# Optimization experiments

Hardware: AMD Instinct MI355X
Metric: run time of the kernel (lower is better)

Reference implementation:

```python
import jax, jax.numpy as jnp
import numpy as np
import math

B, S = 2, 2048
D_IN = 512
D_OUT = 512
P = 8
K = 8


def setup_inputs() -> dict:
    key = jax.random.key(0)
    ks = jax.random.split(key, 8)
    mean_phi = math.log(math.sqrt(2.0 / (D_IN * K)))
    mean_w2 = math.log(math.sqrt(2.0 / D_OUT))
    x = jax.random.normal(ks[0], (B, S, D_IN), dtype=jnp.float32)
    phi_raw = mean_phi + 0.2 * jax.random.normal(ks[1], (D_OUT, D_IN * K), dtype=jnp.float32)
    phi_bias = jnp.zeros((D_OUT,), dtype=jnp.float32)
    raw_weight2 = mean_w2 + 0.2 * jax.random.normal(ks[2], (P, D_OUT, D_OUT), dtype=jnp.float32)
    bias2 = jnp.zeros((P, D_OUT), dtype=jnp.float32)
    gate_raw2 = jnp.full((P,), -3.0, dtype=jnp.float32)
    # kaiming_uniform with a=sqrt(5) on shape (P, 2*D_in, D_out): fan_in = 2*D_in
    bound = math.sqrt(6.0 / ((1.0 + 5.0) * (2 * D_IN)))
    z_weight = jax.random.uniform(ks[3], (P, 2 * D_IN, D_OUT), dtype=jnp.float32,
                                  minval=-bound, maxval=bound)
    gate_raw = jnp.full((P,), -3.0, dtype=jnp.float32)
    output_bias = jnp.zeros((P, D_OUT), dtype=jnp.float32)
    return {
        "x": x, "phi_raw": phi_raw, "phi_bias": phi_bias,
        "raw_weight2": raw_weight2, "bias2": bias2, "gate_raw2": gate_raw2,
        "z_weight": z_weight, "gate_raw": gate_raw, "output_bias": output_bias,
    }


def reference(x, phi_raw, phi_bias, raw_weight2, bias2, gate_raw2,
              z_weight, gate_raw, output_bias):
    sp = jax.nn.softplus
    orig = x.shape
    x_flat = x.reshape(-1, D_IN)                              # [N, Din]
    N = x_flat.shape[0]
    shifts = jnp.linspace(-1.0, 1.0, K, dtype=x.dtype)        # [k]
    phi = sp(x_flat[:, :, None] + shifts[None, None, :])      # [N, Din, k]
    phi_flat = phi.reshape(N, D_IN * K)                       # [N, Din*k]
    # PositiveLinearHK: weight = softplus(raw)^2
    w_phi = jnp.square(sp(phi_raw))                           # [Dout, Din*k]
    x_proj = phi_flat @ w_phi.T + phi_bias                    # [N, Dout]
    g1 = jax.nn.sigmoid(gate_raw)[:, None, None]              # [P,1,1]
    z0 = sp(x_proj[None, :, :] * g1)                          # [P, N, Dout]
    w2 = jnp.square(sp(raw_weight2))                          # [P, Dout, Dout]
    # bmm(z0, w2.transpose(1,2)) == einsum over the second Dout axis of w2
    z1 = jnp.einsum('pnd,ped->pne', z0, w2) + bias2[:, None, :]
    g2 = jax.nn.sigmoid(gate_raw2)[:, None, None]
    z1 = sp(z1 * g2)                                          # [P, N, Dout]
    x_res_in = jnp.concatenate([x_flat, x_flat], axis=-1)     # [N, 2*Din]
    x_res = jnp.einsum('nc,pce->pne', x_res_in, z_weight)     # [P, N, Dout]
    z_final = sp(z1 + x_res) + output_bias[:, None, :]        # [P, N, Dout]
    out = jnp.transpose(z_final, (1, 0, 2))                   # [N, P, Dout]
    return out.reshape(tuple(orig[:-1]) + (P, D_OUT))
```

## Files before the change

### kernel.cpp

```cpp
#include <hip/hip_runtime.h>

typedef unsigned short u16;
typedef __attribute__((ext_vector_type(8))) short bf16x8;
typedef __attribute__((ext_vector_type(4))) float floatx4;
typedef __attribute__((ext_vector_type(8))) unsigned short u16x8;
typedef __attribute__((ext_vector_type(4))) unsigned short u16x4;

#define NTOK 4096
#define DDIN 512
#define DDOUT 512
#define NP 8

__device__ __forceinline__ float b2f(u16 b) {
    union { unsigned int u; float f; } v; v.u = ((unsigned int)b) << 16; return v.f;
}
__device__ __forceinline__ u16 f2b(float f) {
    union { float f; unsigned int u; } v; v.f = f;
    unsigned int r = (v.u + 0x7fffu + ((v.u >> 16) & 1u)) >> 16;
    return (u16)r;
}
__device__ __forceinline__ float sp(float x) {
    return fmaxf(x, 0.f) + __logf(1.f + __expf(-fabsf(x)));
}
__device__ __forceinline__ float sigm(float x) { return 1.f / (1.f + __expf(-x)); }

__device__ __forceinline__ void gld16(const u16* g, u16* l) {
    __builtin_amdgcn_global_load_lds((const __attribute__((address_space(1))) void*)g,
                                     (__attribute__((address_space(3))) void*)l, 16, 0, 0);
}

__global__ void prep_sqsp2(const float* __restrict__ in1, u16* __restrict__ out1, int n1,
                           const float* __restrict__ in2, u16* __restrict__ out2, int n2) {
    int i = blockIdx.x * 256 + threadIdx.x;
    if (i < n1) {
        float s = sp(in1[i]);
        out1[i] = f2b(s * s);
    } else if (i - n1 < n2) {
        int j = i - n1;
        float s = sp(in2[j]);
        out2[j] = f2b(s * s);
    }
}

__global__ void prep_zwT(const float* __restrict__ zw, u16* __restrict__ zwT) {
    int p = blockIdx.z;
    int c0 = blockIdx.x * 32, e0 = blockIdx.y * 32;
    __shared__ float tb[32][33];
    int tx = threadIdx.x, ty = threadIdx.y;
    const float* base = zw + (size_t)p * 1024 * 512;
#pragma unroll
    for (int r = 0; r < 4; ++r) {
        int cl = ty * 4 + r;
        float a = base[(size_t)(c0 + cl) * 512 + e0 + tx];
        float b = base[(size_t)(c0 + cl + 512) * 512 + e0 + tx];
        tb[cl][tx] = a + b;
    }
    __syncthreads();
    u16* outb = zwT + (size_t)p * 512 * 512;
#pragma unroll
    for (int r = 0; r < 4; ++r) {
        int el = ty * 4 + r;
        outb[(size_t)(e0 + el) * 512 + c0 + tx] = f2b(tb[tx][el]);
    }
}

__global__ void phi_kernel(const float* __restrict__ x, u16* __restrict__ phi,
                           u16* __restrict__ xb) {
    int i = blockIdx.x * 256 + threadIdx.x;
    float xv = x[i];
    xb[i] = f2b(xv);
    u16x8 v;
#pragma unroll
    for (int k = 0; k < 8; ++k) {
        float s = -1.f + (2.f / 7.f) * (float)k;
        v[k] = f2b(sp(xv + s));
    }
    *(u16x8*)(phi + (size_t)i * 8) = v;
}


__launch_bounds__(256, 3)
__global__ void gemm1p(const u16* __restrict__ phi, const u16* __restrict__ wphi,
                       u16* __restrict__ xpart) {
    __shared__ __align__(16) u16 lds[2 * 8192];
    u16* As = lds;
    u16* Bs = lds + 8192;

    const int id = blockIdx.x;
    const int kc = id & 7;
    const int local = id >> 3;
    const int o0 = (local & 3) * 128;
    const int n0 = (local >> 2) * 128;
    const int kbase = kc * 512;

    const int t = threadIdx.x;
    const int wave = t >> 6, lane = t & 63;
    const int wm = wave >> 1, wn = wave & 1;
    const int l15 = lane & 15, quad = lane >> 4;
    const int srow = t >> 3;
    const int sgx = (((t & 7) ^ (srow & 7))) * 8;

    floatx4 acc[4][4];
#pragma unroll
    for (int i = 0; i < 4; ++i)
#pragma unroll
        for (int j = 0; j < 4; ++j) acc[i][j] = {0.f, 0.f, 0.f, 0.f};

    for (int k0 = 0; k0 < 512; k0 += 64) {
        const u16* ga = phi + (size_t)(n0 + srow) * 4096 + kbase + k0 + sgx;
        const u16* gb = wphi + (size_t)(o0 + srow) * 4096 + kbase + k0 + sgx;
        __syncthreads();
#pragma unroll
        for (int c = 0; c < 4; ++c) {
            gld16(ga + (size_t)c * 32 * 4096, As + c * 2048 + t * 8);
            gld16(gb + (size_t)c * 32 * 4096, Bs + c * 2048 + t * 8);
        }
        __syncthreads();
#pragma unroll
        for (int ks = 0; ks < 2; ++ks) {
            bf16x8 a[4], b[4];
#pragma unroll
            for (int s = 0; s < 4; ++s) {
                int ra = wm * 64 + s * 16 + l15;
                int rb = wn * 64 + s * 16 + l15;
                a[s] = *(const bf16x8*)(As + ra * 64 + (((ks * 4 + quad) ^ (ra & 7)) * 8));
                b[s] = *(const bf16x8*)(Bs + rb * 64 + (((ks * 4 + quad) ^ (rb & 7)) * 8));
            }
#pragma unroll
            for (int sm = 0; sm < 4; ++sm)
#pragma unroll
                for (int sn = 0; sn < 4; ++sn)
                    acc[sm][sn] = __builtin_amdgcn_mfma_f32_16x16x32_bf16(a[sm], b[sn], acc[sm][sn], 0, 0, 0);
        }
    }

    u16* xp = xpart + (size_t)kc * NTOK * DDOUT;
#pragma unroll
    for (int sm = 0; sm < 4; ++sm)
#pragma unroll
        for (int sn = 0; sn < 4; ++sn) {
            int gcol = o0 + wn * 64 + sn * 16 + l15;
#pragma unroll
            for (int r = 0; r < 4; ++r) {
                int grow = n0 + wm * 64 + sm * 16 + quad * 4 + r;
                xp[(size_t)grow * DDOUT + gcol] = f2b(acc[sm][sn][r]);
            }
        }
}

__global__ void reduce_ep(const u16* __restrict__ xpart, const float* __restrict__ phi_bias,
                          const float* __restrict__ gate_raw, u16* __restrict__ z0) {
    int idx = blockIdx.x * 256 + threadIdx.x;
    int n = idx >> 7;
    int o4 = (idx & 127) * 4;
    size_t base = (size_t)n * DDOUT + o4;
    float s0 = 0.f, s1 = 0.f, s2 = 0.f, s3 = 0.f;
#pragma unroll
    for (int kc = 0; kc < 8; ++kc) {
        u16x4 v = *(const u16x4*)(xpart + (size_t)kc * NTOK * DDOUT + base);
        s0 += b2f(v[0]); s1 += b2f(v[1]); s2 += b2f(v[2]); s3 += b2f(v[3]);
    }
    floatx4 pb = *(const floatx4*)(phi_bias + o4);
    s0 += pb[0]; s1 += pb[1]; s2 += pb[2]; s3 += pb[3];
#pragma unroll
    for (int p = 0; p < NP; ++p) {
        float g = sigm(gate_raw[p]);
        u16x4 v;
        v[0] = f2b(sp(s0 * g)); v[1] = f2b(sp(s1 * g));
        v[2] = f2b(sp(s2 * g)); v[3] = f2b(sp(s3 * g));
        *(u16x4*)(z0 + (size_t)p * NTOK * DDOUT + base) = v;
    }
}

__launch_bounds__(256, 2)
__global__ void gemm23(const u16* __restrict__ z0, const u16* __restrict__ w2b,
                       const u16* __restrict__ xb, const u16* __restrict__ zwT,
                       const float* __restrict__ bias2, const float* __restrict__ gate_raw2,
                       const float* __restrict__ output_bias, float* __restrict__ out) {
    __shared__ __align__(16) u16 lds[4 * 8192];
    u16* A1 = lds;
    u16* B1 = lds + 8192;
    u16* A2 = lds + 16384;
    u16* B2 = lds + 24576;

    const int id = blockIdx.x;
    const int p = id & 7;
    const int local = id >> 3;
    const int e0 = (local & 3) * 128;
    const int n0 = (local >> 2) * 128;

    const int t = threadIdx.x;
    const int wave = t >> 6, lane = t & 63;
    const int wm = wave >> 1, wn = wave & 1;
    const int l15 = lane & 15, quad = lane >> 4;
    const int srow = t >> 3;
    const int sgx = (((t & 7) ^ (srow & 7))) * 8;

    const u16* z0p = z0 + (size_t)p * NTOK * DDOUT;
    const u16* w2p = w2b + (size_t)p * DDOUT * DDOUT;
    const u16* zwp = zwT + (size_t)p * DDOUT * DDIN;

    floatx4 acc1[4][4], acc2[4][4];
#pragma unroll
    for (int i = 0; i < 4; ++i)
#pragma unroll
        for (int j = 0; j < 4; ++j) {
            acc1[i][j] = {0.f, 0.f, 0.f, 0.f};
            acc2[i][j] = {0.f, 0.f, 0.f, 0.f};
        }

    for (int k0 = 0; k0 < 512; k0 += 64) {
        const u16* ga1 = z0p + (size_t)(n0 + srow) * 512 + k0 + sgx;
        const u16* gb1 = w2p + (size_t)(e0 + srow) * 512 + k0 + sgx;
        const u16* ga2 = xb  + (size_t)(n0 + srow) * 512 + k0 + sgx;
        const u16* gb2 = zwp + (size_t)(e0 + srow) * 512 + k0 + sgx;
        __syncthreads();
#pragma unroll
        for (int c = 0; c < 4; ++c) {
            gld16(ga1 + (size_t)c * 32 * 512, A1 + c * 2048 + t * 8);
            gld16(gb1 + (size_t)c * 32 * 512, B1 + c * 2048 + t * 8);
            gld16(ga2 + (size_t)c * 32 * 512, A2 + c * 2048 + t * 8);
            gld16(gb2 + (size_t)c * 32 * 512, B2 + c * 2048 + t * 8);
        }
        __syncthreads();
#pragma unroll
        for (int ks = 0; ks < 2; ++ks) {
            bf16x8 a1[4], b1[4], a2[4], b2[4];
#pragma unroll
            for (int s = 0; s < 4; ++s) {
                int ra = wm * 64 + s * 16 + l15;
                int rb = wn * 64 + s * 16 + l15;
                int ko = ((ks * 4 + quad) ^ (ra & 7)) * 8;
                a1[s] = *(const bf16x8*)(A1 + ra * 64 + ko);
                b1[s] = *(const bf16x8*)(B1 + rb * 64 + ko);
                a2[s] = *(const bf16x8*)(A2 + ra * 64 + ko);
                b2[s] = *(const bf16x8*)(B2 + rb * 64 + ko);
            }
#pragma unroll
            for (int sm = 0; sm < 4; ++sm)
#pragma unroll
                for (int sn = 0; sn < 4; ++sn) {
                    acc1[sm][sn] = __builtin_amdgcn_mfma_f32_16x16x32_bf16(a1[sm], b1[sn], acc1[sm][sn], 0, 0, 0);
                    acc2[sm][sn] = __builtin_amdgcn_mfma_f32_16x16x32_bf16(a2[sm], b2[sn], acc2[sm][sn], 0, 0, 0);
                }
        }
    }

    const float g2p = sigm(gate_raw2[p]);
#pragma unroll
    for (int sm = 0; sm < 4; ++sm)
#pragma unroll
        for (int sn = 0; sn < 4; ++sn) {
            int gcol = e0 + wn * 64 + sn * 16 + l15;
            float bb = bias2[p * DDOUT + gcol];
            float ob = output_bias[p * DDOUT + gcol];
#pragma unroll
            for (int r = 0; r < 4; ++r) {
                int grow = n0 + wm * 64 + sm * 16 + quad * 4 + r;
                float v1 = acc1[sm][sn][r] + bb;
                float o = sp(sp(v1 * g2p) + acc2[sm][sn][r]) + ob;
                out[(size_t)grow * (NP * DDOUT) + p * DDOUT + gcol] = o;
            }
        }
}

extern "C" void kernel_launch(void* const* d_in, const int* in_sizes, int n_in,
                              void* d_out, int out_size, void* d_ws, size_t ws_size,
                              hipStream_t stream) {
    const float* x           = (const float*)d_in[0];
    const float* phi_raw     = (const float*)d_in[1];
    const float* phi_bias    = (const float*)d_in[2];
    const float* raw_weight2 = (const float*)d_in[3];
    const float* bias2       = (const float*)d_in[4];
    const float* gate_raw2   = (const float*)d_in[5];
    const float* z_weight    = (const float*)d_in[6];
    const float* gate_raw    = (const float*)d_in[7];
    const float* output_bias = (const float*)d_in[8];
    float* out = (float*)d_out;

    u16* ws   = (u16*)d_ws;
    u16* phi  = ws;
    u16* wphi = phi + (size_t)4096 * 4096;
    u16* w2b  = wphi + (size_t)512 * 4096;
    u16* zwT  = w2b + (size_t)8 * 512 * 512;
    u16* z0   = zwT + (size_t)8 * 512 * 512;
    u16* xb   = z0 + (size_t)8 * 4096 * 512;
    u16* xpart = (u16*)d_out;

    const int n1 = 512 * 4096, n2 = 8 * 512 * 512;
    hipLaunchKernelGGL(prep_sqsp2, dim3((n1 + n2) / 256), dim3(256), 0, stream,
                       phi_raw, wphi, n1, raw_weight2, w2b, n2);
    hipLaunchKernelGGL(prep_zwT, dim3(16, 16, 8), dim3(32, 8), 0, stream, z_weight, zwT);
    hipLaunchKernelGGL(phi_kernel, dim3(8192), dim3(256), 0, stream, x, phi, xb);
    hipLaunchKernelGGL(gemm1p, dim3(1024), dim3(256), 0, stream, phi, wphi, xpart);
    hipLaunchKernelGGL(reduce_ep, dim3(2048), dim3(256), 0, stream, xpart, phi_bias, gate_raw, z0);
    hipLaunchKernelGGL(gemm23, dim3(1024), dim3(256), 0, stream,
                       z0, w2b, xb, zwT, bias2, gate_raw2, output_bias, out);
}
```

Baseline: 206.9 us.

## Double-buffer LDS in both GEMMs, use 8-wave blocks, halve gemm1 split-K

Both GEMM kernels now use a two-stage LDS ping-pong. The next K-slice's global-to-LDS loads are issued before the MFMAs on the current slice, which also drops one barrier per iteration. Blocks grow to 512 threads (8 waves), each wave covering a 64x32 sub-tile, so each wave holds fewer accumulators and more waves are available to hide latency. gemm1 goes from split-K 8 to 4 with 512 blocks, which cuts partial-sum writes and reduce traffic. In exchange, LDS per block doubles and fewer blocks may fit per CU.

```diff
diff --git a/kernel.cpp b/kernel.cpp
--- a/kernel.cpp
+++ b/kernel.cpp
@@ -10,6 +10,7 @@
 #define DDIN 512
 #define DDOUT 512
 #define NP 8
+#define SPLITK 4
 
 __device__ __forceinline__ float b2f(u16 b) {
     union { unsigned int u; float f; } v; v.u = ((unsigned int)b) << 16; return v.f;
@@ -79,57 +80,67 @@
 }
 
 
-__launch_bounds__(256, 3)
+__launch_bounds__(512, 4)
 __global__ void gemm1p(const u16* __restrict__ phi, const u16* __restrict__ wphi,
                        u16* __restrict__ xpart) {
-    __shared__ __align__(16) u16 lds[2 * 8192];
-    u16* As = lds;
-    u16* Bs = lds + 8192;
+    __shared__ __align__(16) u16 lds[2 * 2 * 8192];
 
     const int id = blockIdx.x;
-    const int kc = id & 7;
-    const int local = id >> 3;
+    const int kc = id & 3;
+    const int local = id >> 2;
     const int o0 = (local & 3) * 128;
     const int n0 = (local >> 2) * 128;
-    const int kbase = kc * 512;
+    const int kbase = kc * 1024;
 
     const int t = threadIdx.x;
     const int wave = t >> 6, lane = t & 63;
-    const int wm = wave >> 1, wn = wave & 1;
+    const int wm = wave & 1, wn = wave >> 1;
     const int l15 = lane & 15, quad = lane >> 4;
     const int srow = t >> 3;
-    const int sgx = (((t & 7) ^ (srow & 7))) * 8;
-
-    floatx4 acc[4][4];
+    const int sgx = ((t & 7) ^ (srow & 7)) * 8;
+
+    const u16* gA = phi  + (size_t)(n0 + srow) * 4096 + kbase + sgx;
+    const u16* gB = wphi + (size_t)(o0 + srow) * 4096 + kbase + sgx;
+
+    floatx4 acc[4][2];
 #pragma unroll
     for (int i = 0; i < 4; ++i)
 #pragma unroll
-        for (int j = 0; j < 4; ++j) acc[i][j] = {0.f, 0.f, 0.f, 0.f};
-
-    for (int k0 = 0; k0 < 512; k0 += 64) {
-        const u16* ga = phi + (size_t)(n0 + srow) * 4096 + kbase + k0 + sgx;
-        const u16* gb = wphi + (size_t)(o0 + srow) * 4096 + kbase + k0 + sgx;
+        for (int j = 0; j < 2; ++j) acc[i][j] = {0.f, 0.f, 0.f, 0.f};
+
+    auto STAGE = [&](int b, int k0) {
+        u16* L = lds + b * 16384;
+#pragma unroll
+        for (int c = 0; c < 2; ++c) {
+            gld16(gA + k0 + c * 64 * 4096, L + c * 4096 + t * 8);
+            gld16(gB + k0 + c * 64 * 4096, L + 8192 + c * 4096 + t * 8);
+        }
+    };
+
+    STAGE(0, 0);
+    for (int it = 0; it < 16; ++it) {
+        const int cur = it & 1;
         __syncthreads();
-#pragma unroll
-        for (int c = 0; c < 4; ++c) {
-            gld16(ga + (size_t)c * 32 * 4096, As + c * 2048 + t * 8);
-            gld16(gb + (size_t)c * 32 * 4096, Bs + c * 2048 + t * 8);
-        }
-        __syncthreads();
+        if (it < 15) STAGE(cur ^ 1, (it + 1) * 64);
+        const u16* As = lds + cur * 16384;
+        const u16* Bs = As + 8192;
 #pragma unroll
         for (int ks = 0; ks < 2; ++ks) {
-            bf16x8 a[4], b[4];
+            bf16x8 a[4], b[2];
 #pragma unroll
             for (int s = 0; s < 4; ++s) {
                 int ra = wm * 64 + s * 16 + l15;
-                int rb = wn * 64 + s * 16 + l15;
                 a[s] = *(const bf16x8*)(As + ra * 64 + (((ks * 4 + quad) ^ (ra & 7)) * 8));
+            }
+#pragma unroll
+            for (int s = 0; s < 2; ++s) {
+                int rb = wn * 32 + s * 16 + l15;
                 b[s] = *(const bf16x8*)(Bs + rb * 64 + (((ks * 4 + quad) ^ (rb & 7)) * 8));
             }
 #pragma unroll
             for (int sm = 0; sm < 4; ++sm)
 #pragma unroll
-                for (int sn = 0; sn < 4; ++sn)
+                for (int sn = 0; sn < 2; ++sn)
                     acc[sm][sn] = __builtin_amdgcn_mfma_f32_16x16x32_bf16(a[sm], b[sn], acc[sm][sn], 0, 0, 0);
         }
     }
@@ -138,8 +149,8 @@
 #pragma unroll
     for (int sm = 0; sm < 4; ++sm)
 #pragma unroll
-        for (int sn = 0; sn < 4; ++sn) {
-            int gcol = o0 + wn * 64 + sn * 16 + l15;
+        for (int sn = 0; sn < 2; ++sn) {
+            int gcol = o0 + wn * 32 + sn * 16 + l15;
 #pragma unroll
             for (int r = 0; r < 4; ++r) {
                 int grow = n0 + wm * 64 + sm * 16 + quad * 4 + r;
@@ -156,7 +167,7 @@
     size_t base = (size_t)n * DDOUT + o4;
     float s0 = 0.f, s1 = 0.f, s2 = 0.f, s3 = 0.f;
 #pragma unroll
-    for (int kc = 0; kc < 8; ++kc) {
+    for (int kc = 0; kc < SPLITK; ++kc) {
         u16x4 v = *(const u16x4*)(xpart + (size_t)kc * NTOK * DDOUT + base);
         s0 += b2f(v[0]); s1 += b2f(v[1]); s2 += b2f(v[2]); s3 += b2f(v[3]);
     }
@@ -172,16 +183,12 @@
     }
 }
 
-__launch_bounds__(256, 2)
+__launch_bounds__(512, 2)
 __global__ void gemm23(const u16* __restrict__ z0, const u16* __restrict__ w2b,
                        const u16* __restrict__ xb, const u16* __restrict__ zwT,
                        const float* __restrict__ bias2, const float* __restrict__ gate_raw2,
                        const float* __restrict__ output_bias, float* __restrict__ out) {
-    __shared__ __align__(16) u16 lds[4 * 8192];
-    u16* A1 = lds;
-    u16* B1 = lds + 8192;
-    u16* A2 = lds + 16384;
-    u16* B2 = lds + 24576;
+    __shared__ __align__(16) u16 lds[2 * 4 * 8192];
 
     const int id = blockIdx.x;
     const int p = id & 7;
@@ -191,55 +198,66 @@
 
     const int t = threadIdx.x;
     const int wave = t >> 6, lane = t & 63;
-    const int wm = wave >> 1, wn = wave & 1;
+    const int wm = wave & 1, wn = wave >> 1;
     const int l15 = lane & 15, quad = lane >> 4;
     const int srow = t >> 3;
-    const int sgx = (((t & 7) ^ (srow & 7))) * 8;
-
-    const u16* z0p = z0 + (size_t)p * NTOK * DDOUT;
-    const u16* w2p = w2b + (size_t)p * DDOUT * DDOUT;
-    const u16* zwp = zwT + (size_t)p * DDOUT * DDIN;
-
-    floatx4 acc1[4][4], acc2[4][4];
+    const int sgx = ((t & 7) ^ (srow & 7)) * 8;
+
+    const u16* gA1 = z0  + (size_t)p * NTOK * DDOUT + (size_t)(n0 + srow) * 512 + sgx;
+    const u16* gB1 = w2b + (size_t)p * DDOUT * DDOUT + (size_t)(e0 + srow) * 512 + sgx;
+    const u16* gA2 = xb  + (size_t)(n0 + srow) * 512 + sgx;
+    const u16* gB2 = zwT + (size_t)p * DDOUT * DDIN + (size_t)(e0 + srow) * 512 + sgx;
+
+    floatx4 acc1[4][2], acc2[4][2];
 #pragma unroll
     for (int i = 0; i < 4; ++i)
 #pragma unroll
-        for (int j = 0; j < 4; ++j) {
+        for (int j = 0; j < 2; ++j) {
             acc1[i][j] = {0.f, 0.f, 0.f, 0.f};
             acc2[i][j] = {0.f, 0.f, 0.f, 0.f};
         }
 
-    for (int k0 = 0; k0 < 512; k0 += 64) {
-        const u16* ga1 = z0p + (size_t)(n0 + srow) * 512 + k0 + sgx;
-        const u16* gb1 = w2p + (size_t)(e0 + srow) * 512 + k0 + sgx;
-        const u16* ga2 = xb  + (size_t)(n0 + srow) * 512 + k0 + sgx;
-        const u16* gb2 = zwp + (size_t)(e0 + srow) * 512 + k0 + sgx;
+    auto STAGE = [&](int b, int k0) {
+        u16* L = lds + b * 32768;
+#pragma unroll
+        for (int c = 0; c < 2; ++c) {
+            gld16(gA1 + k0 + c * 64 * 512, L + c * 4096 + t * 8);
+            gld16(gB1 + k0 + c * 64 * 512, L + 8192 + c * 4096 + t * 8);
+            gld16(gA2 + k0 + c * 64 * 512, L + 16384 + c * 4096 + t * 8);
+            gld16(gB2 + k0 + c * 64 * 512, L + 24576 + c * 4096 + t * 8);
+        }
+    };
+
+    STAGE(0, 0);
+    for (int it = 0; it < 8; ++it) {
+        const int cur = it & 1;
         __syncthreads();
-#pragma unroll
-        for (int c = 0; c < 4; ++c) {
-            gld16(ga1 + (size_t)c * 32 * 512, A1 + c * 2048 + t * 8);
-            gld16(gb1 + (size_t)c * 32 * 512, B1 + c * 2048 + t * 8);
-            gld16(ga2 + (size_t)c * 32 * 512, A2 + c * 2048 + t * 8);
-            gld16(gb2 + (size_t)c * 32 * 512, B2 + c * 2048 + t * 8);
-        }
-        __syncthreads();
+        if (it < 7) STAGE(cur ^ 1, (it + 1) * 64);
+        const u16* A1 = lds + cur * 32768;
+        const u16* B1 = A1 + 8192;
+        const u16* A2 = A1 + 16384;
+        const u16* B2 = A1 + 24576;
 #pragma unroll
         for (int ks = 0; ks < 2; ++ks) {
-            bf16x8 a1[4], b1[4], a2[4], b2[4];
+            bf16x8 a1[4], b1[2], a2[4], b2[2];
 #pragma unroll
             for (int s = 0; s < 4; ++s) {
                 int ra = wm * 64 + s * 16 + l15;
-                int rb = wn * 64 + s * 16 + l15;
                 int ko = ((ks * 4 + quad) ^ (ra & 7)) * 8;
                 a1[s] = *(const bf16x8*)(A1 + ra * 64 + ko);
+                a2[s] = *(const bf16x8*)(A2 + ra * 64 + ko);
+            }
+#pragma unroll
+            for (int s = 0; s < 2; ++s) {
+                int rb = wn * 32 + s * 16 + l15;
+                int ko = ((ks * 4 + quad) ^ (rb & 7)) * 8;
                 b1[s] = *(const bf16x8*)(B1 + rb * 64 + ko);
-                a2[s] = *(const bf16x8*)(A2 + ra * 64 + ko);
                 b2[s] = *(const bf16x8*)(B2 + rb * 64 + ko);
             }
 #pragma unroll
             for (int sm = 0; sm < 4; ++sm)
 #pragma unroll
-                for (int sn = 0; sn < 4; ++sn) {
+                for (int sn = 0; sn < 2; ++sn) {
                     acc1[sm][sn] = __builtin_amdgcn_mfma_f32_16x16x32_bf16(a1[sm], b1[sn], acc1[sm][sn], 0, 0, 0);
                     acc2[sm][sn] = __builtin_amdgcn_mfma_f32_16x16x32_bf16(a2[sm], b2[sn], acc2[sm][sn], 0, 0, 0);
                 }
@@ -250,8 +268,8 @@
 #pragma unroll
     for (int sm = 0; sm < 4; ++sm)
 #pragma unroll
-        for (int sn = 0; sn < 4; ++sn) {
-            int gcol = e0 + wn * 64 + sn * 16 + l15;
+        for (int sn = 0; sn < 2; ++sn) {
+            int gcol = e0 + wn * 32 + sn * 16 + l15;
             float bb = bias2[p * DDOUT + gcol];
             float ob = output_bias[p * DDOUT + gcol];
 #pragma unroll
@@ -292,8 +310,8 @@
                        phi_raw, wphi, n1, raw_weight2, w2b, n2);
     hipLaunchKernelGGL(prep_zwT, dim3(16, 16, 8), dim3(32, 8), 0, stream, z_weight, zwT);
     hipLaunchKernelGGL(phi_kernel, dim3(8192), dim3(256), 0, stream, x, phi, xb);
-    hipLaunchKernelGGL(gemm1p, dim3(1024), dim3(256), 0, stream, phi, wphi, xpart);
+    hipLaunchKernelGGL(gemm1p, dim3(512), dim3(512), 0, stream, phi, wphi, xpart);
     hipLaunchKernelGGL(reduce_ep, dim3(2048), dim3(256), 0, stream, xpart, phi_bias, gate_raw, z0);
-    hipLaunchKernelGGL(gemm23, dim3(1024), dim3(256), 0, stream,
+    hipLaunchKernelGGL(gemm23, dim3(1024), dim3(512), 0, stream,
                        z0, w2b, xb, zwT, bias2, gate_raw2, output_bias, out);
 }
```

Result: no change. 210.7 us (+1.9%).
